# Optimization experiments

Hardware: AMD Instinct MI355X
Metric: run time of the kernel (lower is better)

The kernel has to match this reference:

```python
import jax, jax.numpy as jnp
import numpy as np

NUM_HEADS = 16


def setup_inputs() -> dict:
    key = jax.random.key(0)
    ks = jax.random.split(key, 6)
    B, S, D = 2, 2048, 1024
    x = jax.random.normal(ks[0], (B, S, D), dtype=jnp.float32)
    # Linear weights stored as [d_in, d_out] so forward is x @ W (qkv_bias=False)
    scale = 1.0 / np.sqrt(D)
    Wq = jax.random.normal(ks[1], (D, D), dtype=jnp.float32) * scale
    Wk = jax.random.normal(ks[2], (D, D), dtype=jnp.float32) * scale
    Wv = jax.random.normal(ks[3], (D, D), dtype=jnp.float32) * scale
    Wo = jax.random.normal(ks[4], (D, D), dtype=jnp.float32) * scale
    bo = jax.random.normal(ks[5], (D,), dtype=jnp.float32) * 0.01
    return {"x": x, "Wq": Wq, "Wk": Wk, "Wv": Wv, "Wo": Wo, "bo": bo}


def reference(x, Wq, Wk, Wv, Wo, bo):
    B, S, D = x.shape
    H = NUM_HEADS
    hd = D // H

    def split_heads(t):  # [B,S,D] -> [B,H,S,hd]
        return t.reshape(B, S, H, hd).transpose(0, 2, 1, 3)

    q = split_heads(x @ Wq)
    k = split_heads(x @ Wk)
    v = split_heads(x @ Wv)

    # full score matrix [B,H,S,S]
    scores = jnp.einsum('bhsd,bhtd->bhst', q, k)
    causal = jnp.triu(jnp.ones((S, S), dtype=bool), k=1)
    scores = jnp.where(causal, -jnp.inf, scores)
    attn = jax.nn.softmax(scores * (hd ** -0.5), axis=-1)
    # dropout p=0.0 -> identity
    out = jnp.einsum('bhst,bhtd->bhsd', attn, v)
    out = out.transpose(0, 2, 1, 3).reshape(B, S, D)
    return out @ Wo + bo
```

## Files before the change

kernel.cpp:

```cpp
#include <hip/hip_runtime.h>

typedef unsigned short ushort_t;
typedef unsigned int uint_t;
typedef __attribute__((ext_vector_type(8))) short short8;
typedef __attribute__((ext_vector_type(4))) float floatx4;

#define S_LEN 2048
#define D_DIM 1024
#define H_NUM 16
#define HD 64

__device__ __forceinline__ float bf2f(ushort_t u) {
    union { uint_t i; float f; } c; c.i = ((uint_t)u) << 16; return c.f;
}
__device__ __forceinline__ ushort_t f2bf(float f) {
    union { float f; uint_t i; } c; c.f = f;
    uint_t r = c.i + 0x7fffu + ((c.i >> 16) & 1u);
    return (ushort_t)(r >> 16);
}

__global__ __launch_bounds__(256, 4) void cast_x_kernel(
        const float* __restrict__ in, ushort_t* __restrict__ out) {
    const int idx = (blockIdx.x * 256 + threadIdx.x) * 4;
    const float4 v = *(const float4*)(in + idx);
    ushort4 o;
    o.x = f2bf(v.x); o.y = f2bf(v.y); o.z = f2bf(v.z); o.w = f2bf(v.w);
    *(ushort4*)(out + idx) = o;
}

__global__ __launch_bounds__(256, 2) void transpose4_kernel(
        const float* __restrict__ W0, const float* __restrict__ W1,
        const float* __restrict__ W2, const float* __restrict__ W3,
        ushort_t* __restrict__ T0, ushort_t* __restrict__ T1,
        ushort_t* __restrict__ T2, ushort_t* __restrict__ T3) {
    const int z = blockIdx.z;
    const float* in  = (z == 0) ? W0 : (z == 1) ? W1 : (z == 2) ? W2 : W3;
    ushort_t*    out = (z == 0) ? T0 : (z == 1) ? T1 : (z == 2) ? T2 : T3;
    __shared__ __align__(16) ushort_t t[64][65];
    const int r0 = blockIdx.y * 64, c0 = blockIdx.x * 64;
    const int tr = threadIdx.x >> 4;
    const int tc = (threadIdx.x & 15) * 4;
#pragma unroll
    for (int i = 0; i < 4; ++i) {
        const int row = tr + i * 16;
        const float4 v = *(const float4*)(in + (size_t)(r0 + row) * D_DIM + c0 + tc);
        t[row][tc + 0] = f2bf(v.x); t[row][tc + 1] = f2bf(v.y);
        t[row][tc + 2] = f2bf(v.z); t[row][tc + 3] = f2bf(v.w);
    }
    __syncthreads();
#pragma unroll
    for (int i = 0; i < 4; ++i) {
        const int n = tr + i * 16;
        ushort4 v;
        v.x = t[tc + 0][n]; v.y = t[tc + 1][n];
        v.z = t[tc + 2][n]; v.w = t[tc + 3][n];
        *(ushort4*)(out + (size_t)(c0 + n) * D_DIM + r0 + tc) = v;
    }
}

__device__ __forceinline__ void gemm_tile(
        const ushort_t* __restrict__ A, const ushort_t* __restrict__ BT,
        const int m0, const int n0,
        ushort_t* As, ushort_t* Bs, floatx4 acc[4][4]) {
    const int tid  = threadIdx.x;
    const int w    = tid >> 6;
    const int wm   = (w >> 1) * 64;
    const int wn   = (w & 1) * 64;
    const int lrow = tid & 15;
    const int kq   = ((tid & 63) >> 4) * 8;

    const int flat0 = tid * 8;
    const int flat1 = (256 + tid) * 8;
    const int row0 = flat0 >> 5, kk0 = flat0 & 31;
    const int row1 = flat1 >> 5, kk1 = flat1 & 31;

    for (int k0 = 0; k0 < D_DIM; k0 += 32) {
        const short8 a0 = *(const short8*)(A  + (size_t)(m0 + row0) * D_DIM + k0 + kk0);
        const short8 b0 = *(const short8*)(BT + (size_t)(n0 + row0) * D_DIM + k0 + kk0);
        const short8 a1 = *(const short8*)(A  + (size_t)(m0 + row1) * D_DIM + k0 + kk1);
        const short8 b1 = *(const short8*)(BT + (size_t)(n0 + row1) * D_DIM + k0 + kk1);
        __syncthreads();
        *(short8*)(As + flat0) = a0; *(short8*)(Bs + flat0) = b0;
        *(short8*)(As + flat1) = a1; *(short8*)(Bs + flat1) = b1;
        __syncthreads();

        short8 av[4], bv[4];
#pragma unroll
        for (int i = 0; i < 4; ++i)
            av[i] = *(const short8*)(As + (wm + i * 16 + lrow) * 32 + kq);
#pragma unroll
        for (int j = 0; j < 4; ++j)
            bv[j] = *(const short8*)(Bs + (wn + j * 16 + lrow) * 32 + kq);
#pragma unroll
        for (int i = 0; i < 4; ++i)
#pragma unroll
            for (int j = 0; j < 4; ++j)
                acc[i][j] = __builtin_amdgcn_mfma_f32_16x16x32_bf16(
                    av[i], bv[j], acc[i][j], 0, 0, 0);
    }
}

__global__ __launch_bounds__(256, 2) void gemm_qkv_kernel(
        const ushort_t* __restrict__ A,
        const ushort_t* __restrict__ WqT, const ushort_t* __restrict__ WkT,
        const ushort_t* __restrict__ WvT,
        ushort_t* __restrict__ Qo, ushort_t* __restrict__ Ko,
        ushort_t* __restrict__ Vo) {
    const ushort_t* BT = (blockIdx.z == 0) ? WqT : (blockIdx.z == 1) ? WkT : WvT;
    ushort_t* C        = (blockIdx.z == 0) ? Qo  : (blockIdx.z == 1) ? Ko  : Vo;
    __shared__ __align__(16) ushort_t As[128 * 32];
    __shared__ __align__(16) ushort_t Bs[128 * 32];
    const int m0 = blockIdx.y * 128, n0 = blockIdx.x * 128;

    floatx4 acc[4][4] = {};
    gemm_tile(A, BT, m0, n0, As, Bs, acc);

    const int tid = threadIdx.x;
    const int w = tid >> 6, wm = (w >> 1) * 64, wn = (w & 1) * 64;
    const int lrow = tid & 15;
    const int rquad = ((tid & 63) >> 4) * 4;
#pragma unroll
    for (int i = 0; i < 4; ++i) {
        const int mbase = m0 + wm + i * 16 + rquad;
#pragma unroll
        for (int j = 0; j < 4; ++j) {
            const int gn = n0 + wn + j * 16 + lrow;
#pragma unroll
            for (int r = 0; r < 4; ++r)
                C[(size_t)(mbase + r) * D_DIM + gn] = f2bf(acc[i][j][r]);
        }
    }
}

__global__ __launch_bounds__(256, 2) void gemm_out_kernel(
        const ushort_t* __restrict__ A, const ushort_t* __restrict__ WoT,
        const float* __restrict__ bias, float* __restrict__ C) {
    __shared__ __align__(16) ushort_t As[128 * 32];
    __shared__ __align__(16) ushort_t Bs[128 * 32];
    const int m0 = blockIdx.y * 128, n0 = blockIdx.x * 128;

    floatx4 acc[4][4] = {};
    gemm_tile(A, WoT, m0, n0, As, Bs, acc);

    const int tid = threadIdx.x;
    const int w = tid >> 6, wm = (w >> 1) * 64, wn = (w & 1) * 64;
    const int lrow = tid & 15;
    const int rquad = ((tid & 63) >> 4) * 4;
#pragma unroll
    for (int i = 0; i < 4; ++i) {
        const int mbase = m0 + wm + i * 16 + rquad;
#pragma unroll
        for (int j = 0; j < 4; ++j) {
            const int gn = n0 + wn + j * 16 + lrow;
            const float badd = bias[gn];
#pragma unroll
            for (int r = 0; r < 4; ++r)
                C[(size_t)(mbase + r) * D_DIM + gn] = acc[i][j][r] + badd;
        }
    }
}

__global__ __launch_bounds__(256, 4) void attn_mfma_kernel(
        const ushort_t* __restrict__ Q, const ushort_t* __restrict__ K,
        const ushort_t* __restrict__ V, ushort_t* __restrict__ O) {
    __shared__ __align__(16) ushort_t Ks[64 * 64];
    __shared__ __align__(16) ushort_t Vt[64 * 64];
    __shared__ __align__(16) ushort_t Ps[4][16 * 64];

    const int bh  = blockIdx.x;
    const int b   = bh >> 4, h = bh & 15;
    const int qt  = 31 - (int)blockIdx.y;
    const int q0  = qt * 64;
    const int tid = threadIdx.x;
    const int wq  = tid >> 6;
    const int lane = tid & 63;
    const int col  = lane & 15;
    const int quad = lane >> 4;
    const int qw0  = q0 + wq * 16;
    const size_t rowbase = (size_t)b * S_LEN;
    const int ch0 = h * HD;
    const int c7 = col & 7;

    short8 aq[2];
#pragma unroll
    for (int kc = 0; kc < 2; ++kc)
        aq[kc] = *(const short8*)(Q + (rowbase + qw0 + col) * D_DIM
                                    + ch0 + kc * 32 + quad * 8);

    floatx4 oacc[4] = {};
    float mrun[4], lrun[4];
#pragma unroll
    for (int r = 0; r < 4; ++r) { mrun[r] = -1e30f; lrun[r] = 0.0f; }

    const int ntiles = qt + 1;
    const int skey = tid >> 2;
    const int schk = tid & 3;
    const int vkp = tid & 31;
    const int vdc = tid >> 5;

    for (int t = 0; t < ntiles; ++t) {
        const int kb = t * 64;
        __syncthreads();
        {
            const ushort_t* kg = K + (rowbase + kb + skey) * D_DIM + ch0 + schk * 16;
            const short8 k0 = *(const short8*)(kg);
            const short8 k1 = *(const short8*)(kg + 8);
            const int sw = skey & 7;
            *(short8*)(Ks + skey * 64 + (((2 * schk) ^ sw) << 3)) = k0;
            *(short8*)(Ks + skey * 64 + (((2 * schk + 1) ^ sw) << 3)) = k1;
        }
        {
            const ushort_t* vg = V + (rowbase + kb + 2 * vkp) * D_DIM + ch0 + vdc * 8;
            const short8 v0 = *(const short8*)(vg);
            const short8 v1 = *(const short8*)(vg + D_DIM);
#pragma unroll
            for (int e = 0; e < 8; ++e) {
                const int d = vdc * 8 + e;
                const uint_t pk = (uint_t)(ushort_t)v0[e] | ((uint_t)(ushort_t)v1[e] << 16);
                *(uint_t*)(Vt + d * 64 + ((2 * vkp) ^ ((d & 7) << 3))) = pk;
            }
        }
        __syncthreads();

        if (kb <= qw0 + 15) {
            floatx4 sa[4] = {};
            __builtin_amdgcn_s_setprio(1);
#pragma unroll
            for (int kc = 0; kc < 2; ++kc)
#pragma unroll
                for (int j = 0; j < 4; ++j) {
                    const short8 bk = *(const short8*)(
                        Ks + (j * 16 + col) * 64 + (((kc * 4 + quad) ^ c7) << 3));
                    sa[j] = __builtin_amdgcn_mfma_f32_16x16x32_bf16(
                        aq[kc], bk, sa[j], 0, 0, 0);
                }
            __builtin_amdgcn_s_setprio(0);

            const bool needmask = (kb + 63 > qw0);
#pragma unroll
            for (int j = 0; j < 4; ++j)
#pragma unroll
                for (int r = 0; r < 4; ++r) {
                    float v = sa[j][r] * 0.125f;
                    if (needmask) {
                        const int row = qw0 + quad * 4 + r;
                        const int key = kb + j * 16 + col;
                        v = (key <= row) ? v : -1e30f;
                    }
                    sa[j][r] = v;
                }
#pragma unroll
            for (int r = 0; r < 4; ++r) {
                float mx = fmaxf(fmaxf(sa[0][r], sa[1][r]),
                                 fmaxf(sa[2][r], sa[3][r]));
                mx = fmaxf(mx, __shfl_xor(mx, 1));
                mx = fmaxf(mx, __shfl_xor(mx, 2));
                mx = fmaxf(mx, __shfl_xor(mx, 4));
                mx = fmaxf(mx, __shfl_xor(mx, 8));
                const float mn = fmaxf(mrun[r], mx);
                const float al = __expf(mrun[r] - mn);
                mrun[r] = mn;
                float rs = 0.0f;
#pragma unroll
                for (int j = 0; j < 4; ++j) {
                    const float p = __expf(sa[j][r] - mn);
                    sa[j][r] = p;
                    rs += p;
                }
                rs += __shfl_xor(rs, 1);
                rs += __shfl_xor(rs, 2);
                rs += __shfl_xor(rs, 4);
                rs += __shfl_xor(rs, 8);
                lrun[r] = lrun[r] * al + rs;
#pragma unroll
                for (int jd = 0; jd < 4; ++jd) oacc[jd][r] *= al;
            }
            {
                ushort_t* pw = Ps[wq];
#pragma unroll
                for (int j = 0; j < 4; ++j)
#pragma unroll
                    for (int r = 0; r < 4; ++r) {
                        const int row = quad * 4 + r;
                        pw[row * 64 + ((j * 16 + col) ^ ((row & 7) << 3))] =
                            f2bf(sa[j][r]);
                    }
            }
            asm volatile("s_waitcnt lgkmcnt(0)" ::: "memory");
            __builtin_amdgcn_s_setprio(1);
#pragma unroll
            for (int kc = 0; kc < 2; ++kc) {
                const short8 ap = *(const short8*)(
                    Ps[wq] + col * 64 + (((kc * 4 + quad) ^ c7) << 3));
#pragma unroll
                for (int jd = 0; jd < 4; ++jd) {
                    const short8 bv = *(const short8*)(
                        Vt + (jd * 16 + col) * 64 + (((kc * 4 + quad) ^ c7) << 3));
                    oacc[jd] = __builtin_amdgcn_mfma_f32_16x16x32_bf16(
                        ap, bv, oacc[jd], 0, 0, 0);
                }
            }
            __builtin_amdgcn_s_setprio(0);
        }
    }

#pragma unroll
    for (int r = 0; r < 4; ++r) {
        const int row = qw0 + quad * 4 + r;
        const float inv = 1.0f / lrun[r];
#pragma unroll
        for (int jd = 0; jd < 4; ++jd)
            O[(rowbase + row) * D_DIM + ch0 + jd * 16 + col] =
                f2bf(oacc[jd][r] * inv);
    }
}

extern "C" void kernel_launch(void* const* d_in, const int* in_sizes, int n_in,
                              void* d_out, int out_size, void* d_ws, size_t ws_size,
                              hipStream_t stream) {
    const float* x  = (const float*)d_in[0];
    const float* Wq = (const float*)d_in[1];
    const float* Wk = (const float*)d_in[2];
    const float* Wv = (const float*)d_in[3];
    const float* Wo = (const float*)d_in[4];
    const float* bo = (const float*)d_in[5];
    float* out = (float*)d_out;

    char* ws = (char*)d_ws;
    const size_t MB = 1024 * 1024;
    ushort_t* xb  = (ushort_t*)(ws + 0 * MB);
    ushort_t* WqT = (ushort_t*)(ws + 8 * MB);
    ushort_t* WkT = (ushort_t*)(ws + 10 * MB);
    ushort_t* WvT = (ushort_t*)(ws + 12 * MB);
    ushort_t* WoT = (ushort_t*)(ws + 14 * MB);
    ushort_t* Qb  = (ushort_t*)(ws + 16 * MB);
    ushort_t* Kb  = (ushort_t*)(ws + 24 * MB);
    ushort_t* Vb  = (ushort_t*)(ws + 32 * MB);
    ushort_t* Ob  = (ushort_t*)(ws + 40 * MB);

    cast_x_kernel<<<4096, 256, 0, stream>>>(x, xb);
    transpose4_kernel<<<dim3(16, 16, 4), 256, 0, stream>>>(
        Wq, Wk, Wv, Wo, WqT, WkT, WvT, WoT);

    gemm_qkv_kernel<<<dim3(8, 32, 3), 256, 0, stream>>>(
        xb, WqT, WkT, WvT, Qb, Kb, Vb);

    attn_mfma_kernel<<<dim3(32, 32), 256, 0, stream>>>(Qb, Kb, Vb, Ob);

    gemm_out_kernel<<<dim3(8, 32), 256, 0, stream>>>(Ob, WoT, bo, out);
}
```

Measured before the change: 219.0 us.

## Persistent attention with atomic work queue, direct-to-LDS GEMM loads, folded Q scale

The attention kernel becomes persistent. A fixed grid of 1536 blocks pulls (q-tile, head) items from a global atomic counter, heaviest causal tiles first, with occupancy raised to 6 blocks. The counter is reset inside the cast kernel. The softmax scale is folded into the Q projection epilogue, and the per-tile row-sum shuffles move to a single reduction at the end. The GEMM tile loader switches to global_load_lds, copying straight from global memory into LDS with no register staging. These changes target tail imbalance from uneven causal work, per-tile ALU work and register pressure. In exchange they add an atomic and two barriers per item, and the GEMM now waits on vmcnt(0) every k-step with no prefetch overlap.

```diff
diff --git a/kernel.cpp b/kernel.cpp
--- a/kernel.cpp
+++ b/kernel.cpp
@@ -19,8 +19,16 @@
     return (ushort_t)(r >> 16);
 }
 
+__device__ __forceinline__ void g2l16(const ushort_t* g, ushort_t* l) {
+    __builtin_amdgcn_global_load_lds(
+        (const __attribute__((address_space(1))) void*)g,
+        (__attribute__((address_space(3))) void*)l, 16, 0, 0);
+}
+
 __global__ __launch_bounds__(256, 4) void cast_x_kernel(
-        const float* __restrict__ in, ushort_t* __restrict__ out) {
+        const float* __restrict__ in, ushort_t* __restrict__ out,
+        uint_t* __restrict__ counter) {
+    if (blockIdx.x == 0 && threadIdx.x == 0) counter[0] = 0;
     const int idx = (blockIdx.x * 256 + threadIdx.x) * 4;
     const float4 v = *(const float4*)(in + idx);
     ushort4 o;
@@ -74,14 +82,18 @@
     const int row0 = flat0 >> 5, kk0 = flat0 & 31;
     const int row1 = flat1 >> 5, kk1 = flat1 & 31;
 
+    const ushort_t* ga0 = A  + (size_t)(m0 + row0) * D_DIM + kk0;
+    const ushort_t* gb0 = BT + (size_t)(n0 + row0) * D_DIM + kk0;
+    const ushort_t* ga1 = A  + (size_t)(m0 + row1) * D_DIM + kk1;
+    const ushort_t* gb1 = BT + (size_t)(n0 + row1) * D_DIM + kk1;
+
     for (int k0 = 0; k0 < D_DIM; k0 += 32) {
-        const short8 a0 = *(const short8*)(A  + (size_t)(m0 + row0) * D_DIM + k0 + kk0);
-        const short8 b0 = *(const short8*)(BT + (size_t)(n0 + row0) * D_DIM + k0 + kk0);
-        const short8 a1 = *(const short8*)(A  + (size_t)(m0 + row1) * D_DIM + k0 + kk1);
-        const short8 b1 = *(const short8*)(BT + (size_t)(n0 + row1) * D_DIM + k0 + kk1);
         __syncthreads();
-        *(short8*)(As + flat0) = a0; *(short8*)(Bs + flat0) = b0;
-        *(short8*)(As + flat1) = a1; *(short8*)(Bs + flat1) = b1;
+        g2l16(ga0 + k0, As + flat0);
+        g2l16(gb0 + k0, Bs + flat0);
+        g2l16(ga1 + k0, As + flat1);
+        g2l16(gb1 + k0, Bs + flat1);
+        asm volatile("s_waitcnt vmcnt(0)" ::: "memory");
         __syncthreads();
 
         short8 av[4], bv[4];
@@ -108,6 +120,7 @@
         ushort_t* __restrict__ Vo) {
     const ushort_t* BT = (blockIdx.z == 0) ? WqT : (blockIdx.z == 1) ? WkT : WvT;
     ushort_t* C        = (blockIdx.z == 0) ? Qo  : (blockIdx.z == 1) ? Ko  : Vo;
+    const float sc     = (blockIdx.z == 0) ? 0.125f : 1.0f;
     __shared__ __align__(16) ushort_t As[128 * 32];
     __shared__ __align__(16) ushort_t Bs[128 * 32];
     const int m0 = blockIdx.y * 128, n0 = blockIdx.x * 128;
@@ -127,7 +140,7 @@
             const int gn = n0 + wn + j * 16 + lrow;
 #pragma unroll
             for (int r = 0; r < 4; ++r)
-                C[(size_t)(mbase + r) * D_DIM + gn] = f2bf(acc[i][j][r]);
+                C[(size_t)(mbase + r) * D_DIM + gn] = f2bf(acc[i][j][r] * sc);
         }
     }
 }
@@ -160,158 +173,167 @@
     }
 }
 
-__global__ __launch_bounds__(256, 4) void attn_mfma_kernel(
+__global__ __launch_bounds__(256, 6) void attn_mfma_kernel(
         const ushort_t* __restrict__ Q, const ushort_t* __restrict__ K,
-        const ushort_t* __restrict__ V, ushort_t* __restrict__ O) {
+        const ushort_t* __restrict__ V, ushort_t* __restrict__ O,
+        uint_t* __restrict__ counter) {
     __shared__ __align__(16) ushort_t Ks[64 * 64];
     __shared__ __align__(16) ushort_t Vt[64 * 64];
     __shared__ __align__(16) ushort_t Ps[4][16 * 64];
-
-    const int bh  = blockIdx.x;
-    const int b   = bh >> 4, h = bh & 15;
-    const int qt  = 31 - (int)blockIdx.y;
-    const int q0  = qt * 64;
+    __shared__ uint_t s_item;
+
     const int tid = threadIdx.x;
     const int wq  = tid >> 6;
     const int lane = tid & 63;
     const int col  = lane & 15;
     const int quad = lane >> 4;
-    const int qw0  = q0 + wq * 16;
-    const size_t rowbase = (size_t)b * S_LEN;
-    const int ch0 = h * HD;
     const int c7 = col & 7;
-
-    short8 aq[2];
-#pragma unroll
-    for (int kc = 0; kc < 2; ++kc)
-        aq[kc] = *(const short8*)(Q + (rowbase + qw0 + col) * D_DIM
-                                    + ch0 + kc * 32 + quad * 8);
-
-    floatx4 oacc[4] = {};
-    float mrun[4], lrun[4];
-#pragma unroll
-    for (int r = 0; r < 4; ++r) { mrun[r] = -1e30f; lrun[r] = 0.0f; }
-
-    const int ntiles = qt + 1;
     const int skey = tid >> 2;
     const int schk = tid & 3;
     const int vkp = tid & 31;
     const int vdc = tid >> 5;
 
-    for (int t = 0; t < ntiles; ++t) {
-        const int kb = t * 64;
+    for (int it = 0; it < 1024; ++it) {
         __syncthreads();
-        {
-            const ushort_t* kg = K + (rowbase + kb + skey) * D_DIM + ch0 + schk * 16;
-            const short8 k0 = *(const short8*)(kg);
-            const short8 k1 = *(const short8*)(kg + 8);
-            const int sw = skey & 7;
-            *(short8*)(Ks + skey * 64 + (((2 * schk) ^ sw) << 3)) = k0;
-            *(short8*)(Ks + skey * 64 + (((2 * schk + 1) ^ sw) << 3)) = k1;
-        }
-        {
-            const ushort_t* vg = V + (rowbase + kb + 2 * vkp) * D_DIM + ch0 + vdc * 8;
-            const short8 v0 = *(const short8*)(vg);
-            const short8 v1 = *(const short8*)(vg + D_DIM);
-#pragma unroll
-            for (int e = 0; e < 8; ++e) {
-                const int d = vdc * 8 + e;
-                const uint_t pk = (uint_t)(ushort_t)v0[e] | ((uint_t)(ushort_t)v1[e] << 16);
-                *(uint_t*)(Vt + d * 64 + ((2 * vkp) ^ ((d & 7) << 3))) = pk;
+        if (tid == 0) s_item = atomicAdd(counter, 1u);
+        __syncthreads();
+        const uint_t item = s_item;
+        if (item >= 1024u) break;
+
+        const int qt = 31 - (int)(item >> 5);
+        const int bh = (int)(item & 31u);
+        const int b  = bh >> 4, h = bh & 15;
+        const int q0 = qt * 64;
+        const int qw0 = q0 + wq * 16;
+        const size_t rowbase = (size_t)b * S_LEN;
+        const int ch0 = h * HD;
+
+        short8 aq[2];
+#pragma unroll
+        for (int kc = 0; kc < 2; ++kc)
+            aq[kc] = *(const short8*)(Q + (rowbase + qw0 + col) * D_DIM
+                                        + ch0 + kc * 32 + quad * 8);
+
+        floatx4 oacc[4] = {};
+        float mrun[4], lrun[4];
+#pragma unroll
+        for (int r = 0; r < 4; ++r) { mrun[r] = -1e30f; lrun[r] = 0.0f; }
+
+        const int ntiles = qt + 1;
+        for (int t = 0; t < ntiles; ++t) {
+            const int kb = t * 64;
+            __syncthreads();
+            {
+                const ushort_t* kg = K + (rowbase + kb + skey) * D_DIM + ch0 + schk * 16;
+                const short8 k0 = *(const short8*)(kg);
+                const short8 k1 = *(const short8*)(kg + 8);
+                const int sw = skey & 7;
+                *(short8*)(Ks + skey * 64 + (((2 * schk) ^ sw) << 3)) = k0;
+                *(short8*)(Ks + skey * 64 + (((2 * schk + 1) ^ sw) << 3)) = k1;
+            }
+            {
+                const ushort_t* vg = V + (rowbase + kb + 2 * vkp) * D_DIM + ch0 + vdc * 8;
+                const short8 v0 = *(const short8*)(vg);
+                const short8 v1 = *(const short8*)(vg + D_DIM);
+#pragma unroll
+                for (int e = 0; e < 8; ++e) {
+                    const int d = vdc * 8 + e;
+                    const uint_t pk = (uint_t)(ushort_t)v0[e] | ((uint_t)(ushort_t)v1[e] << 16);
+                    *(uint_t*)(Vt + d * 64 + ((2 * vkp) ^ ((d & 7) << 3))) = pk;
+                }
+            }
+            __syncthreads();
+
+            if (kb <= qw0 + 15) {
+                floatx4 sa[4] = {};
+                __builtin_amdgcn_s_setprio(1);
+#pragma unroll
+                for (int kc = 0; kc < 2; ++kc)
+#pragma unroll
+                    for (int j = 0; j < 4; ++j) {
+                        const short8 bk = *(const short8*)(
+                            Ks + (j * 16 + col) * 64 + (((kc * 4 + quad) ^ c7) << 3));
+                        sa[j] = __builtin_amdgcn_mfma_f32_16x16x32_bf16(
+                            aq[kc], bk, sa[j], 0, 0, 0);
+                    }
+                __builtin_amdgcn_s_setprio(0);
+
+                const bool needmask = (kb + 63 > qw0);
+                if (needmask) {
+#pragma unroll
+                    for (int j = 0; j < 4; ++j)
+#pragma unroll
+                        for (int r = 0; r < 4; ++r) {
+                            const int row = qw0 + quad * 4 + r;
+                            const int key = kb + j * 16 + col;
+                            if (key > row) sa[j][r] = -1e30f;
+                        }
+                }
+#pragma unroll
+                for (int r = 0; r < 4; ++r) {
+                    float mx = fmaxf(fmaxf(sa[0][r], sa[1][r]),
+                                     fmaxf(sa[2][r], sa[3][r]));
+                    mx = fmaxf(mx, __shfl_xor(mx, 1));
+                    mx = fmaxf(mx, __shfl_xor(mx, 2));
+                    mx = fmaxf(mx, __shfl_xor(mx, 4));
+                    mx = fmaxf(mx, __shfl_xor(mx, 8));
+                    const float mn = fmaxf(mrun[r], mx);
+                    const float al = __expf(mrun[r] - mn);
+                    mrun[r] = mn;
+                    float rs = 0.0f;
+#pragma unroll
+                    for (int j = 0; j < 4; ++j) {
+                        const float p = __expf(sa[j][r] - mn);
+                        sa[j][r] = p;
+                        rs += p;
+                    }
+                    lrun[r] = lrun[r] * al + rs;
+#pragma unroll
+                    for (int jd = 0; jd < 4; ++jd) oacc[jd][r] *= al;
+                }
+                {
+                    ushort_t* pw = Ps[wq];
+#pragma unroll
+                    for (int j = 0; j < 4; ++j)
+#pragma unroll
+                        for (int r = 0; r < 4; ++r) {
+                            const int row = quad * 4 + r;
+                            pw[row * 64 + ((j * 16 + col) ^ ((row & 7) << 3))] =
+                                f2bf(sa[j][r]);
+                        }
+                }
+                asm volatile("s_waitcnt lgkmcnt(0)" ::: "memory");
+                __builtin_amdgcn_s_setprio(1);
+#pragma unroll
+                for (int kc = 0; kc < 2; ++kc) {
+                    const short8 ap = *(const short8*)(
+                        Ps[wq] + col * 64 + (((kc * 4 + quad) ^ c7) << 3));
+#pragma unroll
+                    for (int jd = 0; jd < 4; ++jd) {
+                        const short8 bv = *(const short8*)(
+                            Vt + (jd * 16 + col) * 64 + (((kc * 4 + quad) ^ c7) << 3));
+                        oacc[jd] = __builtin_amdgcn_mfma_f32_16x16x32_bf16(
+                            ap, bv, oacc[jd], 0, 0, 0);
+                    }
+                }
+                __builtin_amdgcn_s_setprio(0);
             }
         }
-        __syncthreads();
-
-        if (kb <= qw0 + 15) {
-            floatx4 sa[4] = {};
-            __builtin_amdgcn_s_setprio(1);
-#pragma unroll
-            for (int kc = 0; kc < 2; ++kc)
-#pragma unroll
-                for (int j = 0; j < 4; ++j) {
-                    const short8 bk = *(const short8*)(
-                        Ks + (j * 16 + col) * 64 + (((kc * 4 + quad) ^ c7) << 3));
-                    sa[j] = __builtin_amdgcn_mfma_f32_16x16x32_bf16(
-                        aq[kc], bk, sa[j], 0, 0, 0);
-                }
-            __builtin_amdgcn_s_setprio(0);
-
-            const bool needmask = (kb + 63 > qw0);
-#pragma unroll
-            for (int j = 0; j < 4; ++j)
-#pragma unroll
-                for (int r = 0; r < 4; ++r) {
-                    float v = sa[j][r] * 0.125f;
-                    if (needmask) {
-                        const int row = qw0 + quad * 4 + r;
-                        const int key = kb + j * 16 + col;
-                        v = (key <= row) ? v : -1e30f;
-                    }
-                    sa[j][r] = v;
-                }
-#pragma unroll
-            for (int r = 0; r < 4; ++r) {
-                float mx = fmaxf(fmaxf(sa[0][r], sa[1][r]),
-                                 fmaxf(sa[2][r], sa[3][r]));
-                mx = fmaxf(mx, __shfl_xor(mx, 1));
-                mx = fmaxf(mx, __shfl_xor(mx, 2));
-                mx = fmaxf(mx, __shfl_xor(mx, 4));
-                mx = fmaxf(mx, __shfl_xor(mx, 8));
-                const float mn = fmaxf(mrun[r], mx);
-                const float al = __expf(mrun[r] - mn);
-                mrun[r] = mn;
-                float rs = 0.0f;
-#pragma unroll
-                for (int j = 0; j < 4; ++j) {
-                    const float p = __expf(sa[j][r] - mn);
-                    sa[j][r] = p;
-                    rs += p;
-                }
-                rs += __shfl_xor(rs, 1);
-                rs += __shfl_xor(rs, 2);
-                rs += __shfl_xor(rs, 4);
-                rs += __shfl_xor(rs, 8);
-                lrun[r] = lrun[r] * al + rs;
-#pragma unroll
-                for (int jd = 0; jd < 4; ++jd) oacc[jd][r] *= al;
-            }
-            {
-                ushort_t* pw = Ps[wq];
-#pragma unroll
-                for (int j = 0; j < 4; ++j)
-#pragma unroll
-                    for (int r = 0; r < 4; ++r) {
-                        const int row = quad * 4 + r;
-                        pw[row * 64 + ((j * 16 + col) ^ ((row & 7) << 3))] =
-                            f2bf(sa[j][r]);
-                    }
-            }
-            asm volatile("s_waitcnt lgkmcnt(0)" ::: "memory");
-            __builtin_amdgcn_s_setprio(1);
-#pragma unroll
-            for (int kc = 0; kc < 2; ++kc) {
-                const short8 ap = *(const short8*)(
-                    Ps[wq] + col * 64 + (((kc * 4 + quad) ^ c7) << 3));
-#pragma unroll
-                for (int jd = 0; jd < 4; ++jd) {
-                    const short8 bv = *(const short8*)(
-                        Vt + (jd * 16 + col) * 64 + (((kc * 4 + quad) ^ c7) << 3));
-                    oacc[jd] = __builtin_amdgcn_mfma_f32_16x16x32_bf16(
-                        ap, bv, oacc[jd], 0, 0, 0);
-                }
-            }
-            __builtin_amdgcn_s_setprio(0);
+
+#pragma unroll
+        for (int r = 0; r < 4; ++r) {
+            float l = lrun[r];
+            l += __shfl_xor(l, 1);
+            l += __shfl_xor(l, 2);
+            l += __shfl_xor(l, 4);
+            l += __shfl_xor(l, 8);
+            const int row = qw0 + quad * 4 + r;
+            const float inv = 1.0f / l;
+#pragma unroll
+            for (int jd = 0; jd < 4; ++jd)
+                O[(rowbase + row) * D_DIM + ch0 + jd * 16 + col] =
+                    f2bf(oacc[jd][r] * inv);
         }
-    }
-
-#pragma unroll
-    for (int r = 0; r < 4; ++r) {
-        const int row = qw0 + quad * 4 + r;
-        const float inv = 1.0f / lrun[r];
-#pragma unroll
-        for (int jd = 0; jd < 4; ++jd)
-            O[(rowbase + row) * D_DIM + ch0 + jd * 16 + col] =
-                f2bf(oacc[jd][r] * inv);
     }
 }
 
@@ -336,16 +358,17 @@
     ushort_t* Qb  = (ushort_t*)(ws + 16 * MB);
     ushort_t* Kb  = (ushort_t*)(ws + 24 * MB);
     ushort_t* Vb  = (ushort_t*)(ws + 32 * MB);
-    ushort_t* Ob  = (ushort_t*)(ws + 40 * MB);
-
-    cast_x_kernel<<<4096, 256, 0, stream>>>(x, xb);
+    ushort_t* Ob  = (ushort_t*)(ws + 0 * MB);
+    uint_t*   cnt = (uint_t*)(ws + 40 * MB);
+
+    cast_x_kernel<<<4096, 256, 0, stream>>>(x, xb, cnt);
     transpose4_kernel<<<dim3(16, 16, 4), 256, 0, stream>>>(
         Wq, Wk, Wv, Wo, WqT, WkT, WvT, WoT);
 
     gemm_qkv_kernel<<<dim3(8, 32, 3), 256, 0, stream>>>(
         xb, WqT, WkT, WvT, Qb, Kb, Vb);
 
-    attn_mfma_kernel<<<dim3(32, 32), 256, 0, stream>>>(Qb, Kb, Vb, Ob);
+    attn_mfma_kernel<<<1536, 256, 0, stream>>>(Qb, Kb, Vb, Ob, cnt);
 
     gemm_out_kernel<<<dim3(8, 32), 256, 0, stream>>>(Ob, WoT, bo, out);
 }
```

After: 367.3 us. +67.7%, slower.
